# Kernel optimization log

Hardware: AMD Instinct MI355X
Metric: run time of the kernel (lower is better)

## Reference

```python
import jax, jax.numpy as jnp
import numpy as np
from jax import lax

K = 5
WIN = (1, 1, K, K)
PAD = ((0, 0), (0, 0), (K // 2, K // 2), (K // 2, K // 2))
T_POOL = 0.9


def _conv(x, w, b, pad, dil=(1, 1), groups=1):
    y = lax.conv_general_dilated(x, w, (1, 1), pad, rhs_dilation=dil,
                                 dimension_numbers=('NCHW', 'OIHW', 'NCHW'),
                                 feature_group_count=groups)
    return y + b[None, :, None, None]


def _cbs(x, w, b):
    # Ultralytics Conv: 1x1 conv + folded-BN bias + SiLU
    return jax.nn.silu(_conv(x, w, b, ((0, 0), (0, 0))))


def _maxpool(x):
    return lax.reduce_window(x, -jnp.inf, lax.max, WIN, (1, 1, 1, 1), PAD)


def _sumpool(x):
    return lax.reduce_window(x, 0.0, lax.add, WIN, (1, 1, 1, 1), PAD)


def _tmaxavg(x):
    # TMaxAvgPool2d: blend of max pool and avg pool with weight T
    return T_POOL * _maxpool(x) + (1.0 - T_POOL) * (_sumpool(x) / (K * K))


def _rwpool(x):
    # RWPool2d: exponentially (response-) weighted pooling over the window
    c = lax.stop_gradient(jnp.max(x))  # constant shift, cancels exactly
    e = jnp.exp(x - c)
    return _sumpool(e * x) / (_sumpool(e) + 1e-6)


def setup_inputs():
    key = jax.random.key(0)
    ks = jax.random.split(key, 16)
    B, C1, H, W = 8, 512, 64, 64
    c_ = C1 // 2   # 256
    c4 = c_ * 4    # 1024
    C2 = 512
    f32 = jnp.float32

    def w(k, shape):
        return jax.random.normal(k, shape, f32) * 0.02

    return {
        'x': jax.random.normal(ks[0], (B, C1, H, W), f32),
        'w_sta': w(ks[1], (c_, C1, 1, 1)), 'b_sta': jnp.zeros((c_,), f32),
        'w_cv1': w(ks[2], (C2, c4, 1, 1)), 'b_cv1': jnp.zeros((C2,), f32),
        'w_cv2': w(ks[3], (C2, c4, 1, 1)), 'b_cv2': jnp.zeros((C2,), f32),
        'w_cvend': w(ks[4], (C2, c4, 1, 1)), 'b_cvend': jnp.zeros((C2,), f32),
        'w_dwh': w(ks[5], (c4, 1, 1, 3)), 'b_dwh': jnp.zeros((c4,), f32),
        'w_dwv': w(ks[6], (c4, 1, 3, 1)), 'b_dwv': jnp.zeros((c4,), f32),
        'w_ddwh': w(ks[7], (c4, 1, 1, 3)), 'b_ddwh': jnp.zeros((c4,), f32),
        'w_ddwv': w(ks[8], (c4, 1, 3, 1)), 'b_ddwv': jnp.zeros((c4,), f32),
        'w_c1': w(ks[9], (c4, c4, 1, 1)), 'b_c1': jnp.zeros((c4,), f32),
    }


def reference(x, w_sta, b_sta, w_cv1, b_cv1, w_cv2, b_cv2, w_cvend, b_cvend,
              w_dwh, b_dwh, w_dwv, b_dwv, w_ddwh, b_ddwh, w_ddwv, b_ddwv,
              w_c1, b_c1):
    x_aux = _cbs(x, w_sta, b_sta)                      # [B, c_, H, W]
    y1 = [x_aux]
    y2 = [x_aux]
    for _ in range(3):                                  # SPPF cascades
        y1.append(_tmaxavg(y1[-1]))
        y2.append(_rwpool(y2[-1]))
    y = jnp.concatenate([
        _cbs(jnp.concatenate(y1, 1), w_cv1, b_cv1),     # [B, c2, H, W]
        _cbs(jnp.concatenate(y2, 1), w_cv2, b_cv2),
    ], 1)                                               # [B, c_*4, H, W]
    C = y.shape[1]
    # LSKA: sequential depthwise convs -> 1x1 -> gating multiply
    a = _conv(y, w_dwh, b_dwh, ((0, 0), (1, 1)), groups=C)
    a = _conv(a, w_dwv, b_dwv, ((1, 1), (0, 0)), groups=C)
    a = _conv(a, w_ddwh, b_ddwh, ((0, 0), (2, 2)), dil=(1, 2), groups=C)
    a = _conv(a, w_ddwv, b_ddwv, ((2, 2), (0, 0)), dil=(2, 1), groups=C)
    a = _conv(a, w_c1, b_c1, ((0, 0), (0, 0)))
    return _cbs(y * a, w_cvend, b_cvend)                # [B, c2, H, W]
```

## Files before the change

### kernel.cpp

```cpp
#include <hip/hip_runtime.h>
#include <math.h>

typedef __attribute__((ext_vector_type(8))) short short8;
typedef __attribute__((ext_vector_type(16))) float floatx16;

__device__ __forceinline__ float silu_f(float v) { return v / (1.0f + expf(-v)); }
__device__ __forceinline__ float bf2f(unsigned short u) {
    unsigned int x = ((unsigned int)u) << 16;
    return __uint_as_float(x);
}
__device__ __forceinline__ unsigned short f2bf(float f) {
    unsigned int u = __float_as_uint(f);
    u += 0x7FFFu + ((u >> 16) & 1u);
    return (unsigned short)(u >> 16);
}

struct BSlots { const unsigned short* p[4]; };

#define APITCH 36
#define BPITCH 18

template <int EPI>
__global__ __launch_bounds__(256, 2)
void gemm_mfma(const unsigned short* __restrict__ Ahp,
               const unsigned short* __restrict__ Alp,
               const unsigned short* __restrict__ Ahp2,
               const unsigned short* __restrict__ Alp2, int ldK,
               BSlots bs, BSlots bs2, long bstride,
               const float* __restrict__ bias, const float* __restrict__ bias2,
               void* __restrict__ outv, int OC,
               const unsigned short* __restrict__ gate, int b0, int K)
{
    __shared__ __align__(16) unsigned short As[2][128 * APITCH];
    __shared__ __align__(16) unsigned int   Bsm[256 * BPITCH];

    const int t  = threadIdx.x;
    const int z  = blockIdx.z;
    const int m0 = blockIdx.y * 128;
    const int n0 = blockIdx.x * 256;

    int mA = m0;
    if (Ahp2 != nullptr && m0 >= 512) {
        Ahp = Ahp2; Alp = Alp2; bias = bias2; bs = bs2; mA = m0 - 512;
    }

    const int am = t >> 1, ahf = t & 1;
    const int bkg = t & 7, bn8 = t >> 3;

    const int w = t >> 6, lane = t & 63;
    const int wm = (w & 1) * 64, wn = (w >> 1) * 128;
    const int lm = lane & 31, q = lane >> 5;

    floatx16 acc[2][4];
#pragma unroll
    for (int i = 0; i < 2; ++i)
#pragma unroll
        for (int j = 0; j < 4; ++j)
#pragma unroll
            for (int r = 0; r < 16; ++r) acc[i][j][r] = 0.0f;

    const unsigned short* Aph = Ahp + (size_t)(mA + am) * ldK + ahf * 16;
    const unsigned short* Apl = Alp + (size_t)(mA + am) * ldK + ahf * 16;

    uint4 ah0, ah1, al0, al1, r0, r1, r2, r3;
    {
        ah0 = *(const uint4*)(Aph);
        ah1 = *(const uint4*)(Aph + 8);
        al0 = *(const uint4*)(Apl);
        al1 = *(const uint4*)(Apl + 8);
        const unsigned short* Bp = bs.p[0] + (size_t)z * bstride
                                 + (size_t)(bkg * 4) * 4096 + n0 + bn8 * 8;
        r0 = *(const uint4*)(Bp);
        r1 = *(const uint4*)(Bp + 4096);
        r2 = *(const uint4*)(Bp + 8192);
        r3 = *(const uint4*)(Bp + 12288);
    }

    for (int k0 = 0; k0 < K; k0 += 32) {
        __syncthreads();

        {
            unsigned short* Ad0 = &As[0][am * APITCH + ahf * 16];
            unsigned short* Ad1 = &As[1][am * APITCH + ahf * 16];
            ((uint2*)Ad0)[0] = *((const uint2*)&ah0);
            ((uint2*)Ad0)[1] = *((const uint2*)&ah0 + 1);
            ((uint2*)Ad0)[2] = *((const uint2*)&ah1);
            ((uint2*)Ad0)[3] = *((const uint2*)&ah1 + 1);
            ((uint2*)Ad1)[0] = *((const uint2*)&al0);
            ((uint2*)Ad1)[1] = *((const uint2*)&al0 + 1);
            ((uint2*)Ad1)[2] = *((const uint2*)&al1);
            ((uint2*)Ad1)[3] = *((const uint2*)&al1 + 1);
        }
        {
            const unsigned int* d0 = (const unsigned int*)&r0;
            const unsigned int* d1 = (const unsigned int*)&r1;
            const unsigned int* d2 = (const unsigned int*)&r2;
            const unsigned int* d3 = (const unsigned int*)&r3;
#pragma unroll
            for (int i = 0; i < 8; ++i) {
                unsigned int sel = (i & 1) ? 0x07060302u : 0x05040100u;
                uint2 pv;
                pv.x = __builtin_amdgcn_perm(d1[i >> 1], d0[i >> 1], sel);
                pv.y = __builtin_amdgcn_perm(d3[i >> 1], d2[i >> 1], sel);
                *(uint2*)&Bsm[(bn8 * 8 + i) * BPITCH + bkg * 2] = pv;
            }
        }
        __syncthreads();

        const int k1 = k0 + 32;
        if (k1 < K) {
            ah0 = *(const uint4*)(Aph + k1);
            ah1 = *(const uint4*)(Aph + k1 + 8);
            al0 = *(const uint4*)(Apl + k1);
            al1 = *(const uint4*)(Apl + k1 + 8);
            const unsigned short* Bp = bs.p[k1 >> 8] + (size_t)z * bstride
                                     + (size_t)((k1 & 255) + bkg * 4) * 4096
                                     + n0 + bn8 * 8;
            r0 = *(const uint4*)(Bp);
            r1 = *(const uint4*)(Bp + 4096);
            r2 = *(const uint4*)(Bp + 8192);
            r3 = *(const uint4*)(Bp + 12288);
        }

#pragma unroll
        for (int s = 0; s < 2; ++s) {
            union { short8 v; uint2 u[2]; } afh[2], afl[2], bfr[4];
#pragma unroll
            for (int i = 0; i < 2; ++i) {
                int rb = (wm + 32 * i + lm) * APITCH + s * 16 + q * 8;
                afh[i].u[0] = *(const uint2*)&As[0][rb];
                afh[i].u[1] = *(const uint2*)&As[0][rb + 4];
                afl[i].u[0] = *(const uint2*)&As[1][rb];
                afl[i].u[1] = *(const uint2*)&As[1][rb + 4];
            }
#pragma unroll
            for (int j = 0; j < 4; ++j) {
                int nb = (wn + 32 * j + lm) * BPITCH + s * 8 + q * 4;
                bfr[j].u[0] = *(const uint2*)&Bsm[nb];
                bfr[j].u[1] = *(const uint2*)&Bsm[nb + 2];
            }
#pragma unroll
            for (int i = 0; i < 2; ++i)
#pragma unroll
                for (int j = 0; j < 4; ++j) {
                    acc[i][j] = __builtin_amdgcn_mfma_f32_32x32x16_bf16(
                        afh[i].v, bfr[j].v, acc[i][j], 0, 0, 0);
                    acc[i][j] = __builtin_amdgcn_mfma_f32_32x32x16_bf16(
                        afl[i].v, bfr[j].v, acc[i][j], 0, 0, 0);
                }
        }
    }

#pragma unroll
    for (int i = 0; i < 2; ++i)
#pragma unroll
        for (int j = 0; j < 4; ++j)
#pragma unroll
            for (int r = 0; r < 16; ++r) {
                int row = wm + 32 * i + (r & 3) + 8 * (r >> 2) + 4 * q;
                int col = n0 + wn + 32 * j + lm;
                int mg  = m0 + row;
                size_t ob = ((size_t)z * OC + mg) * 4096 + col;
                float v = acc[i][j][r] + bias[mA + row];
                if (EPI == 0) {
                    ((unsigned short*)outv)[ob] = f2bf(silu_f(v));
                } else if (EPI == 1) {
                    float g = bf2f(gate[((size_t)(b0 + z) * 1024 + mg) * 4096 + col]);
                    ((unsigned short*)outv)[ob] = f2bf(v * g);
                } else {
                    ((float*)outv)[ob] = silu_f(v);
                }
            }
}

__global__ __launch_bounds__(512, 4)
void pool_casc_both(const unsigned short* __restrict__ in,
                    unsigned short* __restrict__ t1, unsigned short* __restrict__ t2,
                    unsigned short* __restrict__ t3, unsigned short* __restrict__ r1,
                    unsigned short* __restrict__ r2, unsigned short* __restrict__ r3)
{
    __shared__ float ha[4096], hb[4096];
    const size_t base = (size_t)blockIdx.x * 4096;
    const int t    = threadIdx.x;
    const int lane = t & 63;
    const int w    = t >> 6;

    const int il2 = (lane - 2) & 63, il1 = (lane - 1) & 63;
    const int ir1 = (lane + 1) & 63, ir2 = (lane + 2) & 63;
    const bool vl2 = lane >= 2, vl1 = lane >= 1;
    const bool vr1 = lane <= 62, vr2 = lane <= 61;

    float v[8];
#pragma unroll
    for (int k = 0; k < 8; ++k)
        v[k] = bf2f(in[base + (size_t)(w + 8 * k) * 64 + lane]);

#pragma unroll
    for (int s = 0; s < 3; ++s) {
        unsigned short* outp = (s == 0) ? t1 : (s == 1) ? t2 : t3;
#pragma unroll
        for (int k = 0; k < 8; ++k) {
            float c = v[k];
            float a2 = __shfl(c, il2, 64);
            float a1 = __shfl(c, il1, 64);
            float b1 = __shfl(c, ir1, 64);
            float b2 = __shfl(c, ir2, 64);
            float mx = -INFINITY, sm = 0.0f;
            mx = vl2 ? fmaxf(mx, a2) : mx;  sm = vl2 ? (sm + a2) : sm;
            mx = vl1 ? fmaxf(mx, a1) : mx;  sm = vl1 ? (sm + a1) : sm;
            mx = fmaxf(mx, c);              sm = sm + c;
            mx = vr1 ? fmaxf(mx, b1) : mx;  sm = vr1 ? (sm + b1) : sm;
            mx = vr2 ? fmaxf(mx, b2) : mx;  sm = vr2 ? (sm + b2) : sm;
            int r = w + 8 * k;
            ha[r * 64 + lane] = mx;
            hb[r * 64 + lane] = sm;
        }
        __syncthreads();
#pragma unroll
        for (int k = 0; k < 8; ++k) {
            int r = w + 8 * k;
            float mx = -INFINITY, sm = 0.0f;
#pragma unroll
            for (int dy = -2; dy <= 2; ++dy) {
                int rr = r + dy;
                if (0 <= rr && rr < 64) {
                    mx = fmaxf(mx, ha[rr * 64 + lane]);
                    sm += hb[rr * 64 + lane];
                }
            }
            float res = 0.9f * mx + 0.1f * (sm * (1.0f / 25.0f));
            v[k] = res;
            outp[base + (size_t)r * 64 + lane] = f2bf(res);
        }
        __syncthreads();
    }

#pragma unroll
    for (int k = 0; k < 8; ++k)
        v[k] = bf2f(in[base + (size_t)(w + 8 * k) * 64 + lane]);
#pragma unroll
    for (int s = 0; s < 3; ++s) {
        unsigned short* outp = (s == 0) ? r1 : (s == 1) ? r2 : r3;
#pragma unroll
        for (int k = 0; k < 8; ++k) {
            float c = v[k];
            float e = expf(c);
            float ea2 = __shfl(e, il2, 64), ca2 = __shfl(c, il2, 64);
            float ea1 = __shfl(e, il1, 64), ca1 = __shfl(c, il1, 64);
            float eb1 = __shfl(e, ir1, 64), cb1 = __shfl(c, ir1, 64);
            float eb2 = __shfl(e, ir2, 64), cb2 = __shfl(c, ir2, 64);
            float se = 0.0f, sx = 0.0f;
            se = vl2 ? (se + ea2) : se;  sx = vl2 ? (sx + ea2 * ca2) : sx;
            se = vl1 ? (se + ea1) : se;  sx = vl1 ? (sx + ea1 * ca1) : sx;
            se = se + e;                 sx = sx + e * c;
            se = vr1 ? (se + eb1) : se;  sx = vr1 ? (sx + eb1 * cb1) : sx;
            se = vr2 ? (se + eb2) : se;  sx = vr2 ? (sx + eb2 * cb2) : sx;
            int r = w + 8 * k;
            ha[r * 64 + lane] = sx;
            hb[r * 64 + lane] = se;
        }
        __syncthreads();
#pragma unroll
        for (int k = 0; k < 8; ++k) {
            int r = w + 8 * k;
            float se = 0.0f, sx = 0.0f;
#pragma unroll
            for (int dy = -2; dy <= 2; ++dy) {
                int rr = r + dy;
                if (0 <= rr && rr < 64) {
                    sx += ha[rr * 64 + lane];
                    se += hb[rr * 64 + lane];
                }
            }
            float res = sx / (se + 1e-6f);
            v[k] = res;
            outp[base + (size_t)r * 64 + lane] = f2bf(res);
        }
        __syncthreads();
    }
}

__global__ __launch_bounds__(512, 4)
void lska_dw_quad(const unsigned short* __restrict__ Y2b, int b0,
                  const float* __restrict__ wh1, const float* __restrict__ bh1,
                  const float* __restrict__ wv1, const float* __restrict__ bv1,
                  const float* __restrict__ wh2, const float* __restrict__ bh2,
                  const float* __restrict__ wv2, const float* __restrict__ bv2,
                  unsigned short* __restrict__ outq)
{
    __shared__ float bufA[4096], bufB[4096];
    const int bi = blockIdx.x;
    const int zz = bi >> 10, c = bi & 1023;
    const unsigned short* src = Y2b + ((size_t)(b0 + zz) * 1024 + c) * 4096;
    unsigned short* dst = outq + (size_t)bi * 4096;
    const int t = threadIdx.x;
    const int lane = t & 63, w = t >> 6;

    const int il1 = (lane - 1) & 63, ir1 = (lane + 1) & 63;
    const int il2 = (lane - 2) & 63, ir2 = (lane + 2) & 63;
    const bool vl1 = lane >= 1, vr1 = lane <= 62;
    const bool vl2 = lane >= 2, vr2 = lane <= 61;

    const float h1w0 = wh1[c * 3], h1w1 = wh1[c * 3 + 1], h1w2 = wh1[c * 3 + 2], h1b = bh1[c];
    const float v1w0 = wv1[c * 3], v1w1 = wv1[c * 3 + 1], v1w2 = wv1[c * 3 + 2], v1b = bv1[c];
    const float h2w0 = wh2[c * 3], h2w1 = wh2[c * 3 + 1], h2w2 = wh2[c * 3 + 2], h2b = bh2[c];
    const float v2w0 = wv2[c * 3], v2w1 = wv2[c * 3 + 1], v2w2 = wv2[c * 3 + 2], v2b = bv2[c];

    float v[8];
#pragma unroll
    for (int k = 0; k < 8; ++k)
        v[k] = bf2f(src[(size_t)(w + 8 * k) * 64 + lane]);

#pragma unroll
    for (int k = 0; k < 8; ++k) {
        float cv = v[k];
        float cl = __shfl(cv, il1, 64);
        float cr = __shfl(cv, ir1, 64);
        float a = fmaf(h1w1, cv, h1b);
        a = vl1 ? fmaf(h1w0, cl, a) : a;
        a = vr1 ? fmaf(h1w2, cr, a) : a;
        bufA[(w + 8 * k) * 64 + lane] = a;
    }
    __syncthreads();
#pragma unroll
    for (int k = 0; k < 8; ++k) {
        int r = w + 8 * k;
        float a = fmaf(v1w1, bufA[r * 64 + lane], v1b);
        if (r >= 1)  a = fmaf(v1w0, bufA[(r - 1) * 64 + lane], a);
        if (r <= 62) a = fmaf(v1w2, bufA[(r + 1) * 64 + lane], a);
        v[k] = a;
    }
#pragma unroll
    for (int k = 0; k < 8; ++k) {
        float cv = v[k];
        float cl = __shfl(cv, il2, 64);
        float cr = __shfl(cv, ir2, 64);
        float a = fmaf(h2w1, cv, h2b);
        a = vl2 ? fmaf(h2w0, cl, a) : a;
        a = vr2 ? fmaf(h2w2, cr, a) : a;
        bufB[(w + 8 * k) * 64 + lane] = a;
    }
    __syncthreads();
#pragma unroll
    for (int k = 0; k < 8; ++k) {
        int r = w + 8 * k;
        float a = fmaf(v2w1, bufB[r * 64 + lane], v2b);
        if (r >= 2)  a = fmaf(v2w0, bufB[(r - 2) * 64 + lane], a);
        if (r <= 61) a = fmaf(v2w2, bufB[(r + 2) * 64 + lane], a);
        dst[(size_t)r * 64 + lane] = f2bf(a);
    }
}

__global__ void f2bf_vec(const float* __restrict__ in, unsigned short* __restrict__ out)
{
    size_t i = ((size_t)blockIdx.x * 256 + threadIdx.x) * 8;
    float4 v0 = *(const float4*)(in + i);
    float4 v1 = *(const float4*)(in + i + 4);
    uint2 o0, o1;
    o0.x = (unsigned)f2bf(v0.x) | ((unsigned)f2bf(v0.y) << 16);
    o0.y = (unsigned)f2bf(v0.z) | ((unsigned)f2bf(v0.w) << 16);
    o1.x = (unsigned)f2bf(v1.x) | ((unsigned)f2bf(v1.y) << 16);
    o1.y = (unsigned)f2bf(v1.z) | ((unsigned)f2bf(v1.w) << 16);
    *(uint2*)(out + i) = o0;
    *(uint2*)(out + i + 4) = o1;
}

__global__ void wsplit(const float* __restrict__ w, unsigned short* __restrict__ wh,
                       unsigned short* __restrict__ wl)
{
    int i = blockIdx.x * 256 + threadIdx.x;
    float v = w[i];
    unsigned short h = f2bf(v);
    wh[i] = h;
    wl[i] = f2bf(v - bf2f(h));
}

extern "C" void kernel_launch(void* const* d_in, const int* in_sizes, int n_in,
                              void* d_out, int out_size, void* d_ws, size_t ws_size,
                              hipStream_t stream)
{
    const float* x       = (const float*)d_in[0];
    const float* w_sta   = (const float*)d_in[1];
    const float* b_sta   = (const float*)d_in[2];
    const float* w_cv1   = (const float*)d_in[3];
    const float* b_cv1   = (const float*)d_in[4];
    const float* w_cv2   = (const float*)d_in[5];
    const float* b_cv2   = (const float*)d_in[6];
    const float* w_cvend = (const float*)d_in[7];
    const float* b_cvend = (const float*)d_in[8];
    const float* w_dwh   = (const float*)d_in[9];
    const float* b_dwh   = (const float*)d_in[10];
    const float* w_dwv   = (const float*)d_in[11];
    const float* b_dwv   = (const float*)d_in[12];
    const float* w_ddwh  = (const float*)d_in[13];
    const float* b_ddwh  = (const float*)d_in[14];
    const float* w_ddwv  = (const float*)d_in[15];
    const float* b_ddwv  = (const float*)d_in[16];
    const float* w_c1    = (const float*)d_in[17];
    const float* b_c1    = (const float*)d_in[18];
    float* outf = (float*)d_out;
    unsigned short* Y2b = (unsigned short*)d_out;

    unsigned short* WS   = (unsigned short*)d_ws;
    unsigned short* xaux = WS;
    unsigned short* t1   = WS + 8388608;
    unsigned short* t2   = WS + 16777216;
    unsigned short* t3   = WS + 25165824;
    unsigned short* r1   = WS + 33554432;
    unsigned short* r2   = WS + 41943040;
    unsigned short* r3   = WS + 50331648;
    unsigned short* WT   = WS + 58720256;
    unsigned short* xb   = t1;
    unsigned short* a4q  = WS;
    unsigned short* gq8  = WS + 16777216;

    unsigned short* sta_h = WT,           * sta_l = WT + 131072;
    unsigned short* cv1_h = WT + 262144,  * cv1_l = WT + 786432;
    unsigned short* cv2_h = WT + 1310720, * cv2_l = WT + 1835008;
    unsigned short* c1_h  = WT + 2359296, * c1_l  = WT + 3407872;
    unsigned short* cve_h = WT + 4456448, * cve_l = WT + 4980736;

    dim3 blk(256);

    f2bf_vec<<<8192, blk, 0, stream>>>(x, xb);
    wsplit<<<512,  blk, 0, stream>>>(w_sta,   sta_h, sta_l);
    wsplit<<<2048, blk, 0, stream>>>(w_cv1,   cv1_h, cv1_l);
    wsplit<<<2048, blk, 0, stream>>>(w_cv2,   cv2_h, cv2_l);
    wsplit<<<4096, blk, 0, stream>>>(w_c1,    c1_h,  c1_l);
    wsplit<<<2048, blk, 0, stream>>>(w_cvend, cve_h, cve_l);

    {
        BSlots s; s.p[0] = xb; s.p[1] = xb + 1048576; s.p[2] = xb; s.p[3] = xb;
        gemm_mfma<0><<<dim3(16, 2, 8), blk, 0, stream>>>(
            sta_h, sta_l, nullptr, nullptr, 512, s, s, 2097152L,
            b_sta, nullptr, xaux, 256, nullptr, 0, 512);
    }

    pool_casc_both<<<2048, dim3(512), 0, stream>>>(xaux, t1, t2, t3, r1, r2, r3);

    {
        BSlots s1; s1.p[0] = xaux; s1.p[1] = t1; s1.p[2] = t2; s1.p[3] = t3;
        BSlots s2; s2.p[0] = xaux; s2.p[1] = r1; s2.p[2] = r2; s2.p[3] = r3;
        gemm_mfma<0><<<dim3(16, 8, 8), blk, 0, stream>>>(
            cv1_h, cv1_l, cv2_h, cv2_l, 1024, s1, s2, 1048576L,
            b_cv1, b_cv2, Y2b, 1024, nullptr, 0, 1024);
    }

    for (int qd = 0; qd < 2; ++qd) {
        const int b0 = 4 * qd;
        lska_dw_quad<<<4096, dim3(512), 0, stream>>>(Y2b, b0,
                                               w_dwh, b_dwh, w_dwv, b_dwv,
                                               w_ddwh, b_ddwh, w_ddwv, b_ddwv, a4q);
        {
            BSlots s; s.p[0] = a4q; s.p[1] = a4q + 1048576;
            s.p[2] = a4q + 2097152; s.p[3] = a4q + 3145728;
            gemm_mfma<1><<<dim3(16, 8, 4), blk, 0, stream>>>(
                c1_h, c1_l, nullptr, nullptr, 1024, s, s, 4194304L,
                b_c1, nullptr, gq8 + (size_t)qd * 16777216, 1024, Y2b, b0, 1024);
        }
    }
    {
        BSlots s; s.p[0] = gq8; s.p[1] = gq8 + 1048576;
        s.p[2] = gq8 + 2097152; s.p[3] = gq8 + 3145728;
        gemm_mfma<2><<<dim3(16, 4, 8), blk, 0, stream>>>(
            cve_h, cve_l, nullptr, nullptr, 1024, s, s, 4194304L,
            b_cvend, nullptr, outf, 512, nullptr, 0, 1024);
    }
}
```

Baseline: 761.6 us.

## Double-buffer LDS tiles in MFMA GEMM with one barrier per k-step

```diff
diff --git a/kernel.cpp b/kernel.cpp
--- a/kernel.cpp
+++ b/kernel.cpp
@@ -31,8 +31,8 @@
                void* __restrict__ outv, int OC,
                const unsigned short* __restrict__ gate, int b0, int K)
 {
-    __shared__ __align__(16) unsigned short As[2][128 * APITCH];
-    __shared__ __align__(16) unsigned int   Bsm[256 * BPITCH];
+    __shared__ __align__(16) unsigned short As[2][2][128 * APITCH];
+    __shared__ __align__(16) unsigned int   Bsm[2][256 * BPITCH];
 
     const int t  = threadIdx.x;
     const int z  = blockIdx.z;
@@ -63,6 +63,7 @@
     const unsigned short* Apl = Alp + (size_t)(mA + am) * ldK + ahf * 16;
 
     uint4 ah0, ah1, al0, al1, r0, r1, r2, r3;
+
     {
         ah0 = *(const uint4*)(Aph);
         ah1 = *(const uint4*)(Aph + 8);
@@ -75,13 +76,84 @@
         r2 = *(const uint4*)(Bp + 8192);
         r3 = *(const uint4*)(Bp + 12288);
     }
-
+    {
+        unsigned short* Ad0 = &As[0][0][am * APITCH + ahf * 16];
+        unsigned short* Ad1 = &As[0][1][am * APITCH + ahf * 16];
+        ((uint2*)Ad0)[0] = *((const uint2*)&ah0);
+        ((uint2*)Ad0)[1] = *((const uint2*)&ah0 + 1);
+        ((uint2*)Ad0)[2] = *((const uint2*)&ah1);
+        ((uint2*)Ad0)[3] = *((const uint2*)&ah1 + 1);
+        ((uint2*)Ad1)[0] = *((const uint2*)&al0);
+        ((uint2*)Ad1)[1] = *((const uint2*)&al0 + 1);
+        ((uint2*)Ad1)[2] = *((const uint2*)&al1);
+        ((uint2*)Ad1)[3] = *((const uint2*)&al1 + 1);
+        const unsigned int* d0 = (const unsigned int*)&r0;
+        const unsigned int* d1 = (const unsigned int*)&r1;
+        const unsigned int* d2 = (const unsigned int*)&r2;
+        const unsigned int* d3 = (const unsigned int*)&r3;
+#pragma unroll
+        for (int i = 0; i < 8; ++i) {
+            unsigned int sel = (i & 1) ? 0x07060302u : 0x05040100u;
+            uint2 pv;
+            pv.x = __builtin_amdgcn_perm(d1[i >> 1], d0[i >> 1], sel);
+            pv.y = __builtin_amdgcn_perm(d3[i >> 1], d2[i >> 1], sel);
+            *(uint2*)&Bsm[0][(bn8 * 8 + i) * BPITCH + bkg * 2] = pv;
+        }
+    }
+    if (32 < K) {
+        ah0 = *(const uint4*)(Aph + 32);
+        ah1 = *(const uint4*)(Aph + 40);
+        al0 = *(const uint4*)(Apl + 32);
+        al1 = *(const uint4*)(Apl + 40);
+        const unsigned short* Bp = bs.p[0] + (size_t)z * bstride
+                                 + (size_t)(32 + bkg * 4) * 4096 + n0 + bn8 * 8;
+        r0 = *(const uint4*)(Bp);
+        r1 = *(const uint4*)(Bp + 4096);
+        r2 = *(const uint4*)(Bp + 8192);
+        r3 = *(const uint4*)(Bp + 12288);
+    }
+    __syncthreads();
+
+    int cur = 0;
     for (int k0 = 0; k0 < K; k0 += 32) {
-        __syncthreads();
-
-        {
-            unsigned short* Ad0 = &As[0][am * APITCH + ahf * 16];
-            unsigned short* Ad1 = &As[1][am * APITCH + ahf * 16];
+        const unsigned short* A0 = &As[cur][0][0];
+        const unsigned short* A1 = &As[cur][1][0];
+        const unsigned int*   Bc = &Bsm[cur][0];
+        __builtin_amdgcn_s_setprio(1);
+#pragma unroll
+        for (int s = 0; s < 2; ++s) {
+            union { short8 v; uint2 u[2]; } afh[2], afl[2], bfr[4];
+#pragma unroll
+            for (int i = 0; i < 2; ++i) {
+                int rb = (wm + 32 * i + lm) * APITCH + s * 16 + q * 8;
+                afh[i].u[0] = *(const uint2*)&A0[rb];
+                afh[i].u[1] = *(const uint2*)&A0[rb + 4];
+                afl[i].u[0] = *(const uint2*)&A1[rb];
+                afl[i].u[1] = *(const uint2*)&A1[rb + 4];
+            }
+#pragma unroll
+            for (int j = 0; j < 4; ++j) {
+                int nb = (wn + 32 * j + lm) * BPITCH + s * 8 + q * 4;
+                bfr[j].u[0] = *(const uint2*)&Bc[nb];
+                bfr[j].u[1] = *(const uint2*)&Bc[nb + 2];
+            }
+#pragma unroll
+            for (int i = 0; i < 2; ++i)
+#pragma unroll
+                for (int j = 0; j < 4; ++j) {
+                    acc[i][j] = __builtin_amdgcn_mfma_f32_32x32x16_bf16(
+                        afh[i].v, bfr[j].v, acc[i][j], 0, 0, 0);
+                    acc[i][j] = __builtin_amdgcn_mfma_f32_32x32x16_bf16(
+                        afl[i].v, bfr[j].v, acc[i][j], 0, 0, 0);
+                }
+        }
+        __builtin_amdgcn_s_setprio(0);
+
+        const int k1 = k0 + 32;
+        if (k1 < K) {
+            const int nxt = cur ^ 1;
+            unsigned short* Ad0 = &As[nxt][0][am * APITCH + ahf * 16];
+            unsigned short* Ad1 = &As[nxt][1][am * APITCH + ahf * 16];
             ((uint2*)Ad0)[0] = *((const uint2*)&ah0);
             ((uint2*)Ad0)[1] = *((const uint2*)&ah0 + 1);
             ((uint2*)Ad0)[2] = *((const uint2*)&ah1);
@@ -90,8 +162,6 @@
             ((uint2*)Ad1)[1] = *((const uint2*)&al0 + 1);
             ((uint2*)Ad1)[2] = *((const uint2*)&al1);
             ((uint2*)Ad1)[3] = *((const uint2*)&al1 + 1);
-        }
-        {
             const unsigned int* d0 = (const unsigned int*)&r0;
             const unsigned int* d1 = (const unsigned int*)&r1;
             const unsigned int* d2 = (const unsigned int*)&r2;
@@ -102,53 +172,25 @@
                 uint2 pv;
                 pv.x = __builtin_amdgcn_perm(d1[i >> 1], d0[i >> 1], sel);
                 pv.y = __builtin_amdgcn_perm(d3[i >> 1], d2[i >> 1], sel);
-                *(uint2*)&Bsm[(bn8 * 8 + i) * BPITCH + bkg * 2] = pv;
+                *(uint2*)&Bsm[nxt][(bn8 * 8 + i) * BPITCH + bkg * 2] = pv;
+            }
+            const int k2 = k0 + 64;
+            if (k2 < K) {
+                ah0 = *(const uint4*)(Aph + k2);
+                ah1 = *(const uint4*)(Aph + k2 + 8);
+                al0 = *(const uint4*)(Apl + k2);
+                al1 = *(const uint4*)(Apl + k2 + 8);
+                const unsigned short* Bp = bs.p[k2 >> 8] + (size_t)z * bstride
+                                         + (size_t)((k2 & 255) + bkg * 4) * 4096
+                                         + n0 + bn8 * 8;
+                r0 = *(const uint4*)(Bp);
+                r1 = *(const uint4*)(Bp + 4096);
+                r2 = *(const uint4*)(Bp + 8192);
+                r3 = *(const uint4*)(Bp + 12288);
             }
         }
         __syncthreads();
-
-        const int k1 = k0 + 32;
-        if (k1 < K) {
-            ah0 = *(const uint4*)(Aph + k1);
-            ah1 = *(const uint4*)(Aph + k1 + 8);
-            al0 = *(const uint4*)(Apl + k1);
-            al1 = *(const uint4*)(Apl + k1 + 8);
-            const unsigned short* Bp = bs.p[k1 >> 8] + (size_t)z * bstride
-                                     + (size_t)((k1 & 255) + bkg * 4) * 4096
-                                     + n0 + bn8 * 8;
-            r0 = *(const uint4*)(Bp);
-            r1 = *(const uint4*)(Bp + 4096);
-            r2 = *(const uint4*)(Bp + 8192);
-            r3 = *(const uint4*)(Bp + 12288);
-        }
-
-#pragma unroll
-        for (int s = 0; s < 2; ++s) {
-            union { short8 v; uint2 u[2]; } afh[2], afl[2], bfr[4];
-#pragma unroll
-            for (int i = 0; i < 2; ++i) {
-                int rb = (wm + 32 * i + lm) * APITCH + s * 16 + q * 8;
-                afh[i].u[0] = *(const uint2*)&As[0][rb];
-                afh[i].u[1] = *(const uint2*)&As[0][rb + 4];
-                afl[i].u[0] = *(const uint2*)&As[1][rb];
-                afl[i].u[1] = *(const uint2*)&As[1][rb + 4];
-            }
-#pragma unroll
-            for (int j = 0; j < 4; ++j) {
-                int nb = (wn + 32 * j + lm) * BPITCH + s * 8 + q * 4;
-                bfr[j].u[0] = *(const uint2*)&Bsm[nb];
-                bfr[j].u[1] = *(const uint2*)&Bsm[nb + 2];
-            }
-#pragma unroll
-            for (int i = 0; i < 2; ++i)
-#pragma unroll
-                for (int j = 0; j < 4; ++j) {
-                    acc[i][j] = __builtin_amdgcn_mfma_f32_32x32x16_bf16(
-                        afh[i].v, bfr[j].v, acc[i][j], 0, 0, 0);
-                    acc[i][j] = __builtin_amdgcn_mfma_f32_32x32x16_bf16(
-                        afl[i].v, bfr[j].v, acc[i][j], 0, 0, 0);
-                }
-        }
+        cur ^= 1;
     }
 
 #pragma unroll
```

Result: slower. 811.4 us (+6.5%).
